# Kernel optimization log

Hardware: AMD Instinct MI355X
Metric: run time of the kernel (lower is better)

The kernel has to match this reference:

```python
import jax, jax.numpy as jnp
import numpy as np
from jax import lax

LN_EPS = 1e-5
GRN_EPS = 1e-6


def _convnext_block(x, cw, cb, lng, lnb, w1, b1, gg, gb, w2, b2):
    # x: [B, C, H, W] NCHW; cw: [C, 1, 7, 7] depthwise kernel
    dim = x.shape[1]
    y = lax.conv_general_dilated(
        x, cw, window_strides=(1, 1), padding=[(3, 3), (3, 3)],
        dimension_numbers=('NCHW', 'OIHW', 'NCHW'), feature_group_count=dim)
    y = y + cb[None, :, None, None]
    y = y.transpose(0, 2, 3, 1)  # NHWC
    # LayerNorm over channels
    mu = y.mean(-1, keepdims=True)
    var = ((y - mu) ** 2).mean(-1, keepdims=True)
    y = (y - mu) * lax.rsqrt(var + LN_EPS) * lng + lnb
    # pointwise expand
    y = y @ w1 + b1
    y = jax.nn.gelu(y, approximate=False)
    # Global Response Normalization
    gx = jnp.sqrt(jnp.sum(y * y, axis=(1, 2), keepdims=True))  # [B,1,1,C']
    nx = gx / (gx.mean(-1, keepdims=True) + GRN_EPS)
    y = gg * (y * nx) + gb + y
    # pointwise project
    y = y @ w2 + b2
    return y.transpose(0, 3, 1, 2) + x


def _stack_blocks(x, cw, cb, lng, lnb, w1, b1, gg, gb, w2, b2):
    for i in range(cw.shape[0]):
        x = _convnext_block(x, cw[i], cb[i], lng[i], lnb[i], w1[i], b1[i],
                            gg[i], gb[i], w2[i], b2[i])
    return x


def setup_inputs() -> dict:
    key = jax.random.key(0)
    B, C, H, W = 8, 256, 64, 64
    K = 1024
    INTER = 4 * C
    DEPTH = 2
    ks = jax.random.split(key, 8)
    x = jax.random.normal(ks[0], (B, C, H, W), jnp.float32)
    codebook = jax.random.uniform(ks[1], (K, C), jnp.float32, -1.0 / K, 1.0 / K)

    def make_params(k):
        k1, k2, k3 = jax.random.split(k, 3)
        return dict(
            conv_w=0.02 * jax.random.normal(k1, (DEPTH, C, 1, 7, 7), jnp.float32),
            conv_b=jnp.zeros((DEPTH, C), jnp.float32),
            ln_g=jnp.ones((DEPTH, C), jnp.float32),
            ln_b=jnp.zeros((DEPTH, C), jnp.float32),
            fc1_w=0.02 * jax.random.normal(k2, (DEPTH, C, INTER), jnp.float32),
            fc1_b=jnp.zeros((DEPTH, INTER), jnp.float32),
            grn_g=jnp.zeros((DEPTH, INTER), jnp.float32),
            grn_b=jnp.zeros((DEPTH, INTER), jnp.float32),
            fc2_w=0.02 * jax.random.normal(k3, (DEPTH, INTER, C), jnp.float32),
            fc2_b=jnp.zeros((DEPTH, C), jnp.float32),
        )

    enc = make_params(ks[2])
    dec = make_params(ks[3])
    out = {'x': x, 'codebook': codebook}
    for name, p in (('enc', enc), ('dec', dec)):
        for k2, v in p.items():
            out[f'{name}_{k2}'] = v
    return out


def reference(x, codebook,
              enc_conv_w, enc_conv_b, enc_ln_g, enc_ln_b, enc_fc1_w, enc_fc1_b,
              enc_grn_g, enc_grn_b, enc_fc2_w, enc_fc2_b,
              dec_conv_w, dec_conv_b, dec_ln_g, dec_ln_b, dec_fc1_w, dec_fc1_b,
              dec_grn_g, dec_grn_b, dec_fc2_w, dec_fc2_b):
    B, C, H, W = x.shape
    inputs = _stack_blocks(x, enc_conv_w, enc_conv_b, enc_ln_g, enc_ln_b,
                           enc_fc1_w, enc_fc1_b, enc_grn_g, enc_grn_b,
                           enc_fc2_w, enc_fc2_b)
    inputs = inputs.transpose(0, 2, 3, 1)  # [B,H,W,C]
    flat = inputs.reshape(-1, C)  # [N, C]
    # squared Euclidean distances (argmin invariant to sqrt)
    d2 = (jnp.sum(flat * flat, axis=1, keepdims=True)
          - 2.0 * (flat @ codebook.T)
          + jnp.sum(codebook * codebook, axis=1)[None, :])  # [N, K]
    encoding_indices = jnp.argmin(d2, axis=1)  # [N]
    quantized = codebook[encoding_indices].reshape(inputs.shape)  # [B,H,W,C]
    matched_indices = encoding_indices.reshape(B, H, W)
    # straight-through estimator
    quantized = lax.stop_gradient(quantized) + inputs - lax.stop_gradient(inputs)
    quantized = quantized.transpose(0, 3, 1, 2)  # [B,C,H,W]
    decoded = _stack_blocks(quantized, dec_conv_w, dec_conv_b, dec_ln_g, dec_ln_b,
                            dec_fc1_w, dec_fc1_b, dec_grn_g, dec_grn_b,
                            dec_fc2_w, dec_fc2_b)
    return quantized, decoded, matched_indices
```

## Files before the change

kernel.cpp:

```cpp
#include <hip/hip_runtime.h>
#include <math.h>
#include <stdint.h>

typedef unsigned short u16;
typedef unsigned long long u64;
typedef __attribute__((ext_vector_type(8))) short bf16x8;
typedef __attribute__((ext_vector_type(4))) float f32x4;

__device__ __forceinline__ u16 bfhi(float v) {
  unsigned u = __float_as_uint(v);
  u += 0x7FFFu + ((u >> 16) & 1u);
  return (u16)(u >> 16);
}
__device__ __forceinline__ float b2f(u16 h) { return __uint_as_float((unsigned)h << 16); }

__device__ __forceinline__ void gload16(void* lds, const void* g) {
  __builtin_amdgcn_global_load_lds(
      (const __attribute__((address_space(1))) unsigned int*)g,
      (__attribute__((address_space(3))) unsigned int*)lds, 16, 0, 0);
}

__global__ __launch_bounds__(256) void k_conv(const float* __restrict__ in,
                                              const float* __restrict__ cw,
                                              const float* __restrict__ cb,
                                              float* __restrict__ out) {
  const int bx = blockIdx.x;
  const int c = bx & 255;
  __shared__ float patch[70 * 76];
  const int t = threadIdx.x;
  const float* plane = in + (size_t)bx * 4096;
  for (int i = t; i < 1330; i += 256) {
    const int row = i / 19, cf = i - row * 19;
    const int bit = (row >> 2) & 1;
    const int gf = cf - 1 - bit;
    const int h = row - 3;
    float4 v = {0.f, 0.f, 0.f, 0.f};
    if ((unsigned)h < 64u && (unsigned)gf < 16u) v = *(const float4*)(plane + h * 64 + gf * 4);
    *(float4*)(patch + row * 76 + cf * 4) = v;
  }
  const float* wp = cw + c * 49;
  float wt[49];
#pragma unroll
  for (int i = 0; i < 49; ++i) wt[i] = wp[i];
  const float bias = cb[c];
  __syncthreads();
  const int j = t & 7, i = t >> 3;
  const int w0 = j * 8, h0 = i * 2;
  float acc[2][8];
#pragma unroll
  for (int dr = 0; dr < 2; ++dr)
#pragma unroll
    for (int ww = 0; ww < 8; ++ww) acc[dr][ww] = bias;
#pragma unroll
  for (int r = 0; r < 8; ++r) {
    const int prow = h0 + r;
    const int bit = (prow >> 2) & 1;
    const float* base = patch + prow * 76 + w0 + 4 * bit;
    float win[16];
#pragma unroll
    for (int q = 0; q < 4; ++q) {
      const float4 v = *(const float4*)(base + q * 4);
      win[q * 4 + 0] = v.x; win[q * 4 + 1] = v.y;
      win[q * 4 + 2] = v.z; win[q * 4 + 3] = v.w;
    }
#pragma unroll
    for (int dr = 0; dr < 2; ++dr) {
      const int kh = r - dr;
      if (kh >= 0 && kh < 7) {
#pragma unroll
        for (int kw = 0; kw < 7; ++kw) {
          const float wv = wt[kh * 7 + kw];
#pragma unroll
          for (int ww = 0; ww < 8; ++ww)
            acc[dr][ww] = fmaf(win[ww + kw + 1], wv, acc[dr][ww]);
        }
      }
    }
  }
  float* op = out + (size_t)bx * 4096;
#pragma unroll
  for (int dr = 0; dr < 2; ++dr) {
    const int hh = h0 + dr;
    float4 o1, o2;
    o1.x = acc[dr][0]; o1.y = acc[dr][1]; o1.z = acc[dr][2]; o1.w = acc[dr][3];
    o2.x = acc[dr][4]; o2.y = acc[dr][5]; o2.z = acc[dr][6]; o2.w = acc[dr][7];
    *(float4*)(op + hh * 64 + w0) = o1;
    *(float4*)(op + hh * 64 + w0 + 4) = o2;
  }
}

__global__ __launch_bounds__(256) void k_lnT(const float* __restrict__ src,
                                             const float* __restrict__ g,
                                             const float* __restrict__ bt,
                                             u16* __restrict__ Rh, u16* __restrict__ Rl,
                                             const int wlo) {
  __shared__ float T[256 * 33];
  __shared__ float red[8 * 32];
  __shared__ float gs[256], bs[256];
  const int t = threadIdx.x;
  const int n0 = blockIdx.x * 32;
  const int b = n0 >> 12, pl = n0 & 4095;
  gs[t] = g[t];
  bs[t] = bt[t];
  const int m = t & 7, h = t >> 3;
  const float* sp = src + (((size_t)(b * 256)) << 12) + pl + m * 4;
#pragma unroll
  for (int it = 0; it < 8; ++it) {
    const int c = it * 32 + h;
    const float4 v = *(const float4*)(sp + ((size_t)c << 12));
    *(float4*)(T + c * 33 + m * 4) = v;
  }
  __syncthreads();
  const int p = t & 31, qq = t >> 5;
  float s = 0.f;
#pragma unroll
  for (int jj = 0; jj < 32; ++jj) s += T[(qq * 32 + jj) * 33 + p];
  red[qq * 32 + p] = s;
  __syncthreads();
  float tot = 0.f;
#pragma unroll
  for (int k = 0; k < 8; ++k) tot += red[k * 32 + p];
  const float mu = tot * (1.0f / 256.0f);
  __syncthreads();
  float s2 = 0.f;
#pragma unroll
  for (int jj = 0; jj < 32; ++jj) {
    const float d = T[(qq * 32 + jj) * 33 + p] - mu;
    s2 = fmaf(d, d, s2);
  }
  red[qq * 32 + p] = s2;
  __syncthreads();
  float tot2 = 0.f;
#pragma unroll
  for (int k = 0; k < 8; ++k) tot2 += red[k * 32 + p];
  const float rs = 1.0f / sqrtf(tot2 * (1.0f / 256.0f) + 1e-5f);
#pragma unroll
  for (int jj = 0; jj < 32; ++jj) {
    const int c = qq * 32 + jj;
    const float y = (T[c * 33 + p] - mu) * rs * gs[c] + bs[c];
    const u16 hh = bfhi(y);
    const u16 ll = bfhi(y - b2f(hh));
    ((unsigned*)T)[c * 33 + p] = ((unsigned)hh << 16) | ll;
  }
  __syncthreads();
  const int w = t >> 6, l = t & 63;
  const unsigned* Tu = (const unsigned*)T;
#pragma unroll
  for (int r = 0; r < 4; ++r) {
    const int px = r * 8 + w * 2 + (l >> 5);
    const int c0 = (l & 31) * 8;
    unsigned hp[4], lp[4];
#pragma unroll
    for (int jj = 0; jj < 4; ++jj) {
      const unsigned a = Tu[(c0 + 2 * jj) * 33 + px];
      const unsigned bb = Tu[(c0 + 2 * jj + 1) * 33 + px];
      hp[jj] = (a >> 16) | (bb & 0xffff0000u);
      lp[jj] = (a & 0xffffu) | (bb << 16);
    }
    const size_t base = (size_t)(n0 + px) * 256 + c0;
    *(uint4*)(Rh + base) = make_uint4(hp[0], hp[1], hp[2], hp[3]);
    if (wlo) *(uint4*)(Rl + base) = make_uint4(lp[0], lp[1], lp[2], lp[3]);
  }
}

template <int KD, int SPLIT, int EPI>
__global__ __launch_bounds__(256) void k_gemm(
    const u16* __restrict__ Ah_, const u16* __restrict__ Al_,
    const u16* __restrict__ Bh_, const u16* __restrict__ Bl_,
    const int row0, const long long bstride,
    const float* __restrict__ pbias,
    u16* __restrict__ poh, u16* __restrict__ pol,
    float* __restrict__ pxout, const float* __restrict__ pxin,
    float* __restrict__ pgx2, u64* __restrict__ pmin) {
  constexpr int STAGE_B = (SPLIT ? 4 : 2) * 16384;
  constexpr int TRANS_B = (EPI == 1) ? 64 * 129 * 4 : 0;
  constexpr int SMEM_B = STAGE_B > TRANS_B ? STAGE_B : TRANS_B;
  __shared__ __align__(16) char smem[SMEM_B];
  u16* As_h = (u16*)smem;
  u16* As_l = (u16*)(smem + 16384);
  u16* Bs_h = (u16*)(smem + (SPLIT ? 32768 : 16384));
  u16* Bs_l = (u16*)(smem + 49152);

  const int t = threadIdx.x;
  const int w = t >> 6, l = t & 63;
  const int quad = l >> 4, lm = l & 15;
  const int wr = (w & 1) * 64, wc = (w >> 1) * 64;
  const int colt = blockIdx.x, rowt = blockIdx.y;
  const int nblk0 = rowt * 128;
  const int bglob = (row0 + nblk0) >> 12;

  const u16* Agh = Ah_ + (size_t)nblk0 * KD;
  const u16* Agl = SPLIT ? (Al_ + (size_t)nblk0 * KD) : Ah_;
  const u16* Bgh = Bh_ + (size_t)bglob * (size_t)bstride + (size_t)(colt * 128) * KD;
  const u16* Bgl = SPLIT ? (Bl_ + (size_t)bglob * (size_t)bstride + (size_t)(colt * 128) * KD) : Bh_;

  f32x4 acc[4][4];
  const f32x4 zz = {0.f, 0.f, 0.f, 0.f};
#pragma unroll
  for (int i = 0; i < 4; ++i)
#pragma unroll
    for (int j = 0; j < 4; ++j) acc[i][j] = zz;

  auto stage = [&](u16* Sp, const u16* Gp, int ks) {
#pragma unroll
    for (int ii = 0; ii < 4; ++ii) {
      const int o = ii * 4096 + t * 16;
      const int row = o >> 7;
      const int kl = (((o >> 4) & 7) ^ (row & 7)) << 3;
      gload16((char*)Sp + o, Gp + (size_t)row * KD + ks * 64 + kl);
    }
  };

#pragma unroll 1
  for (int ks = 0; ks < KD / 64; ++ks) {
    stage(As_h, Agh, ks);
    stage(Bs_h, Bgh, ks);
    if constexpr (SPLIT) {
      stage(As_l, Agl, ks);
      stage(Bs_l, Bgl, ks);
    }
    __syncthreads();
#pragma unroll
    for (int kk = 0; kk < 2; ++kk) {
      bf16x8 ah[4], bh[4];
#pragma unroll
      for (int i = 0; i < 4; ++i) {
        const int row = wr + i * 16 + lm;
        ah[i] = *(const bf16x8*)(As_h + row * 64 + (((kk * 4 + quad) ^ (row & 7)) << 3));
        const int col = wc + i * 16 + lm;
        bh[i] = *(const bf16x8*)(Bs_h + col * 64 + (((kk * 4 + quad) ^ (col & 7)) << 3));
      }
#pragma unroll
      for (int i = 0; i < 4; ++i)
#pragma unroll
        for (int j = 0; j < 4; ++j)
          acc[i][j] = __builtin_amdgcn_mfma_f32_16x16x32_bf16(ah[i], bh[j], acc[i][j], 0, 0, 0);
      if constexpr (SPLIT) {
        bf16x8 xl[4];
#pragma unroll
        for (int i = 0; i < 4; ++i) {
          const int row = wr + i * 16 + lm;
          xl[i] = *(const bf16x8*)(As_l + row * 64 + (((kk * 4 + quad) ^ (row & 7)) << 3));
        }
#pragma unroll
        for (int i = 0; i < 4; ++i)
#pragma unroll
          for (int j = 0; j < 4; ++j)
            acc[i][j] = __builtin_amdgcn_mfma_f32_16x16x32_bf16(xl[i], bh[j], acc[i][j], 0, 0, 0);
#pragma unroll
        for (int i = 0; i < 4; ++i) {
          const int col = wc + i * 16 + lm;
          xl[i] = *(const bf16x8*)(Bs_l + col * 64 + (((kk * 4 + quad) ^ (col & 7)) << 3));
        }
#pragma unroll
        for (int i = 0; i < 4; ++i)
#pragma unroll
          for (int j = 0; j < 4; ++j)
            acc[i][j] = __builtin_amdgcn_mfma_f32_16x16x32_bf16(ah[i], xl[j], acc[i][j], 0, 0, 0);
      }
    }
    __syncthreads();
  }

  if constexpr (EPI == 0) {
    float csum[4] = {0.f, 0.f, 0.f, 0.f};
    float bv[4];
#pragma unroll
    for (int j = 0; j < 4; ++j) bv[j] = pbias[colt * 128 + wc + j * 16 + lm];
#pragma unroll
    for (int i = 0; i < 4; ++i) {
#pragma unroll
      for (int r = 0; r < 4; ++r) {
        const int row = nblk0 + wr + i * 16 + quad * 4 + r;
#pragma unroll
        for (int j = 0; j < 4; ++j) {
          const int col = colt * 128 + wc + j * 16 + lm;
          const float x = acc[i][j][r] + bv[j];
          const float gl = 0.5f * x * (1.0f + erff(x * 0.70710678118654752f));
          csum[j] = fmaf(gl, gl, csum[j]);
          const size_t idx = (size_t)row * 1024 + col;
          const u16 h = bfhi(gl);
          poh[idx] = h;
          if constexpr (SPLIT) pol[idx] = bfhi(gl - b2f(h));
        }
      }
    }
#pragma unroll
    for (int j = 0; j < 4; ++j) {
      float cs = csum[j];
      cs += __shfl_xor(cs, 16);
      cs += __shfl_xor(cs, 32);
      if (quad == 0)
        unsafeAtomicAdd(&pgx2[bglob * 1024 + colt * 128 + wc + j * 16 + lm], cs);
    }
  } else if constexpr (EPI == 1) {
    float* T = (float*)smem;
    const int pg0 = (row0 + nblk0) & 4095;
    const int bb = (row0 + nblk0) >> 12;
#pragma unroll 1
    for (int h = 0; h < 2; ++h) {
      __syncthreads();
      if ((w >> 1) == h) {
#pragma unroll
        for (int i = 0; i < 4; ++i) {
          const int row = wr + i * 16 + quad * 4;
#pragma unroll
          for (int j = 0; j < 4; ++j) {
            const int cl = j * 16 + lm;
#pragma unroll
            for (int r = 0; r < 4; ++r) T[cl * 129 + row + r] = acc[i][j][r];
          }
        }
      }
      __syncthreads();
      const int lp = (l & 31) * 4;
      const int ch2 = l >> 5;
#pragma unroll
      for (int step = 0; step < 8; ++step) {
        const int cl = w * 16 + step * 2 + ch2;
        const int cg = colt * 128 + h * 64 + cl;
        float4 tv = *(float4*)&T[cl * 129 + lp];
        const float bv2 = pbias[cg];
        const size_t nchw = (((size_t)(bb * 256 + cg)) << 12) + pg0 + lp;
        const float4 xv = *(const float4*)(pxin + nchw);
        float4 z;
        z.x = tv.x + bv2 + xv.x;
        z.y = tv.y + bv2 + xv.y;
        z.z = tv.z + bv2 + xv.z;
        z.w = tv.w + bv2 + xv.w;
        if (pxout) *(float4*)(pxout + nchw) = z;
        if (poh) *(float4*)&T[cl * 129 + lp] = z;
      }
      if (poh) {
        __syncthreads();
        const int cl3 = t & 63;
        const int cg3 = colt * 128 + h * 64 + cl3;
        const int r0 = (t >> 6) * 32;
#pragma unroll
        for (int n = 0; n < 32; ++n) {
          const float z = T[cl3 * 129 + r0 + n];
          const size_t idx = (size_t)(nblk0 + r0 + n) * 256 + cg3;
          const u16 hh = bfhi(z);
          poh[idx] = hh;
          pol[idx] = bfhi(z - b2f(hh));
        }
      }
    }
  } else {
#pragma unroll
    for (int i = 0; i < 4; ++i) {
#pragma unroll
      for (int r = 0; r < 4; ++r) {
        const int nloc = nblk0 + wr + i * 16 + quad * 4 + r;
        const float tnv = pxin[nloc];
        u64 best = ~0ULL;
#pragma unroll
        for (int j = 0; j < 4; ++j) {
          const int code = colt * 128 + wc + j * 16 + lm;
          const float d = __fadd_rn(__fsub_rn(tnv, __fmul_rn(2.0f, acc[i][j][r])), pbias[code]);
          const u64 pk = (((u64)__float_as_uint(d)) << 32) | (unsigned)code;
          best = pk < best ? pk : best;
        }
#pragma unroll
        for (int off = 1; off < 16; off <<= 1) {
          unsigned lo32 = (unsigned)best, hi32 = (unsigned)(best >> 32);
          lo32 = __shfl_xor(lo32, off);
          hi32 = __shfl_xor(hi32, off);
          const u64 o2 = (((u64)hi32) << 32) | lo32;
          best = o2 < best ? o2 : best;
        }
        if (lm == 0) atomicMin(pmin + nloc, best);
      }
    }
  }
}

__global__ __launch_bounds__(256) void k_rownorm(const u16* __restrict__ Eh,
                                                 const u16* __restrict__ El,
                                                 float* __restrict__ tn) {
  const int t = threadIdx.x;
  const int r = t >> 2, p = t & 3;
  const int n = blockIdx.x * 64 + r;
  const u16* ph = Eh + (size_t)n * 256 + p * 64;
  const u16* pl = El + (size_t)n * 256 + p * 64;
  float s = 0.f;
#pragma unroll
  for (int j = 0; j < 8; ++j) {
    const uint4 hv = *(const uint4*)(ph + j * 8);
    const uint4 lv = *(const uint4*)(pl + j * 8);
    const unsigned hu[4] = {hv.x, hv.y, hv.z, hv.w};
    const unsigned lu[4] = {lv.x, lv.y, lv.z, lv.w};
#pragma unroll
    for (int q = 0; q < 4; ++q) {
      const float v0 = b2f((u16)(hu[q] & 0xffff)) + b2f((u16)(lu[q] & 0xffff));
      const float v1 = b2f((u16)(hu[q] >> 16)) + b2f((u16)(lu[q] >> 16));
      s = fmaf(v0, v0, s);
      s = fmaf(v1, v1, s);
    }
  }
  s += __shfl_xor(s, 1);
  s += __shfl_xor(s, 2);
  if (p == 0) tn[n] = s;
}

__global__ __launch_bounds__(256) void k_grn_scale(const float* __restrict__ GX2,
                                                   const float* __restrict__ gg,
                                                   float* __restrict__ S, int b0) {
  const int b = b0 + blockIdx.x, t = threadIdx.x;
  const float* gxb = GX2 + (size_t)b * 1024;
  float gx[4];
  float s = 0.f;
#pragma unroll
  for (int i = 0; i < 4; ++i) {
    gx[i] = sqrtf(gxb[t + i * 256]);
    s += gx[i];
  }
  const int w = t >> 6, l = t & 63;
#pragma unroll
  for (int o = 32; o > 0; o >>= 1) s += __shfl_down(s, o);
  __shared__ float red[4];
  __shared__ float bc;
  if (l == 0) red[w] = s;
  __syncthreads();
  if (t == 0) bc = 1.0f / ((red[0] + red[1] + red[2] + red[3]) * (1.0f / 1024.0f) + 1e-6f);
  __syncthreads();
  const float inv = bc;
#pragma unroll
  for (int i = 0; i < 4; ++i)
    S[(size_t)b * 1024 + t + i * 256] = fmaf(gg[t + i * 256], gx[i] * inv, 1.0f);
}

__global__ __launch_bounds__(256) void k_w2prep(const float* __restrict__ W2,
                                                const float* __restrict__ S, int b0,
                                                u16* __restrict__ Wh, u16* __restrict__ Wl) {
  const int bx = blockIdx.x;
  const int b = b0 + (bx >> 8), n = bx & 255;
  const int t = threadIdx.x;
#pragma unroll
  for (int j = 0; j < 4; ++j) {
    const int k = t + j * 256;
    const float v = W2[(size_t)k * 256 + n] * S[(size_t)b * 1024 + k];
    const size_t idx = ((size_t)(b * 256 + n)) * 1024 + k;
    const u16 h = bfhi(v);
    Wh[idx] = h;
    Wl[idx] = bfhi(v - b2f(h));
  }
}

__global__ __launch_bounds__(256) void k_bias2(const float* __restrict__ W2,
                                               const float* __restrict__ gb,
                                               const float* __restrict__ b2,
                                               float* __restrict__ out) {
  const int c = blockIdx.x, t = threadIdx.x;
  float acc = 0.f;
#pragma unroll
  for (int j = 0; j < 4; ++j) {
    const int k = t + j * 256;
    acc = fmaf(gb[k], W2[(size_t)k * 256 + c], acc);
  }
  const int w = t >> 6, l = t & 63;
#pragma unroll
  for (int o = 32; o > 0; o >>= 1) acc += __shfl_down(acc, o);
  __shared__ float red[4];
  if (l == 0) red[w] = acc;
  __syncthreads();
  if (t == 0) out[c] = red[0] + red[1] + red[2] + red[3] + b2[c];
}

__global__ __launch_bounds__(256) void k_wt(const float* __restrict__ W1,
                                            u16* __restrict__ Wh, u16* __restrict__ Wl) {
  const int bx = blockIdx.x;
  const int d = bx >> 10, n = bx & 1023;
  const int k = threadIdx.x;
  const float v = W1[(size_t)d * 262144 + (size_t)k * 1024 + n];
  const size_t idx = (size_t)bx * 256 + k;
  const u16 h = bfhi(v);
  Wh[idx] = h;
  Wl[idx] = bfhi(v - b2f(h));
}

__global__ __launch_bounds__(256) void k_csplit(const float* __restrict__ C,
                                                u16* __restrict__ Ch, u16* __restrict__ Cl) {
  const size_t i = (size_t)blockIdx.x * 256 + threadIdx.x;
  const float v = C[i];
  const u16 h = bfhi(v);
  Ch[i] = h;
  Cl[i] = bfhi(v - b2f(h));
}

__device__ __forceinline__ float np_pairwise_sq_256(const float* p) {
  float half[2];
#pragma unroll
  for (int hh = 0; hh < 2; ++hh) {
    float r[8];
#pragma unroll
    for (int j = 0; j < 8; ++j) {
      const float v = p[hh * 128 + j];
      r[j] = __fmul_rn(v, v);
    }
    for (int i = 8; i < 128; i += 8) {
#pragma unroll
      for (int j = 0; j < 8; ++j) {
        const float v = p[hh * 128 + i + j];
        r[j] = __fadd_rn(r[j], __fmul_rn(v, v));
      }
    }
    half[hh] = __fadd_rn(__fadd_rn(__fadd_rn(r[0], r[1]), __fadd_rn(r[2], r[3])),
                         __fadd_rn(__fadd_rn(r[4], r[5]), __fadd_rn(r[6], r[7])));
  }
  return __fadd_rn(half[0], half[1]);
}

__global__ __launch_bounds__(256) void k_c2(const float* __restrict__ cbk, float* __restrict__ c2) {
  const int k = blockIdx.x * 256 + threadIdx.x;
  c2[k] = np_pairwise_sq_256(cbk + (size_t)k * 256);
}

__global__ __launch_bounds__(256) void k_idx(const u64* __restrict__ pk, float* __restrict__ outI) {
  const int n = blockIdx.x * 256 + threadIdx.x;
  outI[n] = (float)(unsigned)(pk[n] & 0xffffffffULL);
}

__global__ __launch_bounds__(256) void k_gather(const u64* __restrict__ pk,
                                                const float* __restrict__ cbk,
                                                float* __restrict__ outq) {
  const int t = threadIdx.x;
  const int p0 = blockIdx.x * 64;
  const int b = p0 >> 12, pl = (p0 & 4095) + (t & 63);
  const int cg = t >> 6;
  const int n = p0 + (t & 63);
  const int k = (int)(unsigned)(pk[n] & 0xffffffffULL);
  const float* crow = cbk + (size_t)k * 256 + cg * 64;
  float* ob = outq + (((size_t)(b * 256 + cg * 64)) << 12) + pl;
#pragma unroll 1
  for (int j = 0; j < 16; ++j) {
    const float4 cv = *(const float4*)(crow + j * 4);
    ob[((size_t)(j * 4 + 0)) << 12] = cv.x;
    ob[((size_t)(j * 4 + 1)) << 12] = cv.y;
    ob[((size_t)(j * 4 + 2)) << 12] = cv.z;
    ob[((size_t)(j * 4 + 3)) << 12] = cv.w;
  }
}

extern "C" void kernel_launch(void* const* d_in, const int* in_sizes, int n_in,
                              void* d_out, int out_size, void* d_ws, size_t ws_size,
                              hipStream_t stream) {
  const float* x = (const float*)d_in[0];
  const float* cbk = (const float*)d_in[1];
  const float* Pe[10];
  const float* Pd[10];
  for (int i = 0; i < 10; ++i) Pe[i] = (const float*)d_in[2 + i];
  for (int i = 0; i < 10; ++i) Pd[i] = (const float*)d_in[12 + i];

  float* ws = (float*)d_ws;
  size_t o = 0;
  auto alloc = [&](size_t nf) {
    float* p = ws + o;
    o += (nf + 63) & ~(size_t)63;
    return p;
  };
  float* P1 = alloc(8388608);
  u16* Rh = (u16*)alloc(4194304);
  u16* Rl = (u16*)alloc(4194304);
  u16* W1th_e = (u16*)alloc(262144);
  u16* W1tl_e = (u16*)alloc(262144);
  u16* W1th_d = (u16*)alloc(262144);
  u16* W1tl_d = (u16*)alloc(262144);
  u16* W2sh = (u16*)alloc(1048576);
  u16* W2sl = (u16*)alloc(1048576);
  u16* Ch = (u16*)alloc(131072);
  u16* Cl = (u16*)alloc(131072);
  float* C2v = alloc(1024);
  float* GX2 = alloc(8192);
  float* Sv = alloc(8192);
  float* bias2v = alloc(256);
  float* tn = alloc(32768);
  u64* pk = (u64*)alloc(65536);
  const size_t fixedf = o;
  const size_t availf = (ws_size / 4 > fixedf) ? ws_size / 4 - fixedf : 0;
  int chunkB = (int)(availf / 4194304);
  if (chunkB > 8) chunkB = 8;
  if (chunkB < 1) chunkB = 1;
  float* Cv = ws + o;
  u16* Mh = (u16*)(ws + o);
  u16* Ml = (u16*)(ws + o + (size_t)chunkB * 2097152);

  float* outQ = (float*)d_out;
  float* outD = outQ + 8388608;
  float* outI = outD + 8388608;

  auto run_enc = [&](const float* xin, float* xout, u16* Eh, u16* El,
                     const float* const* pp, int d) {
    k_conv<<<2048, 256, 0, stream>>>(xin, pp[0] + (size_t)d * 256 * 49, pp[1] + d * 256, Cv);
    k_lnT<<<1024, 256, 0, stream>>>(Cv, pp[2] + d * 256, pp[3] + d * 256, Rh, Rl, 1);
    k_bias2<<<256, 256, 0, stream>>>(pp[8] + (size_t)d * 262144, pp[7] + d * 1024,
                                     pp[9] + d * 256, bias2v);
    hipMemsetAsync(GX2, 0, 8192 * 4, stream);
    for (int b0 = 0; b0 < 8; b0 += chunkB) {
      const int nb = (8 - b0 < chunkB) ? 8 - b0 : chunkB;
      k_gemm<256, 1, 0><<<dim3(8, nb * 32), 256, 0, stream>>>(
          Rh + (size_t)b0 * 4096 * 256, Rl + (size_t)b0 * 4096 * 256,
          W1th_e + (size_t)d * 262144, W1tl_e + (size_t)d * 262144,
          b0 * 4096, 0, Pe[5] + d * 1024, Mh, Ml, nullptr, nullptr, GX2, nullptr);
      k_grn_scale<<<nb, 256, 0, stream>>>(GX2, pp[6] + d * 1024, Sv, b0);
      k_w2prep<<<nb * 256, 256, 0, stream>>>(pp[8] + (size_t)d * 262144, Sv, b0, W2sh, W2sl);
      k_gemm<1024, 1, 1><<<dim3(2, nb * 32), 256, 0, stream>>>(
          Mh, Ml, W2sh, W2sl, b0 * 4096, 262144LL, bias2v,
          Eh ? Eh + (size_t)b0 * 4096 * 256 : (u16*)nullptr,
          El ? El + (size_t)b0 * 4096 * 256 : (u16*)nullptr,
          xout, xin, nullptr, nullptr);
    }
  };

  auto run_dec = [&](const float* xin, float* xout, const float* const* pp, int d) {
    k_conv<<<2048, 256, 0, stream>>>(xin, pp[0] + (size_t)d * 256 * 49, pp[1] + d * 256, Cv);
    k_lnT<<<1024, 256, 0, stream>>>(Cv, pp[2] + d * 256, pp[3] + d * 256, Rh, Rl, 0);
    k_bias2<<<256, 256, 0, stream>>>(pp[8] + (size_t)d * 262144, pp[7] + d * 1024,
                                     pp[9] + d * 256, bias2v);
    hipMemsetAsync(GX2, 0, 8192 * 4, stream);
    for (int b0 = 0; b0 < 8; b0 += chunkB) {
      const int nb = (8 - b0 < chunkB) ? 8 - b0 : chunkB;
      k_gemm<256, 0, 0><<<dim3(8, nb * 32), 256, 0, stream>>>(
          Rh + (size_t)b0 * 4096 * 256, nullptr,
          W1th_d + (size_t)d * 262144, nullptr,
          b0 * 4096, 0, Pd[5] + d * 1024, Mh, nullptr, nullptr, nullptr, GX2, nullptr);
      k_grn_scale<<<nb, 256, 0, stream>>>(GX2, pp[6] + d * 1024, Sv, b0);
      k_w2prep<<<nb * 256, 256, 0, stream>>>(pp[8] + (size_t)d * 262144, Sv, b0, W2sh, W2sl);
      k_gemm<1024, 0, 1><<<dim3(2, nb * 32), 256, 0, stream>>>(
          Mh, nullptr, W2sh, nullptr, b0 * 4096, 262144LL, bias2v,
          nullptr, nullptr, xout, xin, nullptr, nullptr);
    }
  };

  k_wt<<<2048, 256, 0, stream>>>(Pe[4], W1th_e, W1tl_e);
  k_wt<<<2048, 256, 0, stream>>>(Pd[4], W1th_d, W1tl_d);
  k_csplit<<<1024, 256, 0, stream>>>(cbk, Ch, Cl);
  k_c2<<<4, 256, 0, stream>>>(cbk, C2v);

  run_enc(x, P1, nullptr, nullptr, Pe, 0);
  run_enc(P1, nullptr, Rh, Rl, Pe, 1);

  k_rownorm<<<512, 256, 0, stream>>>(Rh, Rl, tn);
  hipMemsetAsync(pk, 0xFF, 32768 * 8, stream);
  k_gemm<256, 1, 2><<<dim3(8, 256), 256, 0, stream>>>(Rh, Rl, Ch, Cl, 0, 0,
                                                      C2v, nullptr, nullptr, nullptr,
                                                      tn, nullptr, pk);
  k_idx<<<128, 256, 0, stream>>>(pk, outI);
  k_gather<<<512, 256, 0, stream>>>(pk, cbk, outQ);

  run_dec(outQ, P1, Pd, 0);
  run_dec(P1, outD, Pd, 1);
}
```

Before: 1.011 ms.

## Double-buffer GEMM K-loop with 32-wide stages and swizzle block-to-tile mapping

The GEMM main loop moves from single-buffered 64-wide K stages to double-buffered 32-wide stages. Each iteration prefetches the next stage into the alternate LDS buffer while computing on the current one, and drops one barrier per iteration. It also remaps the linear block id so that groups of 8 row tiles share column tiles, aiming for better L2 reuse of the B operand. The change adds a new LDS swizzle for 64-byte rows, which brings a risk of bank conflicts, and halves the MFMA work done between barriers.

```diff
diff --git a/kernel.cpp b/kernel.cpp
--- a/kernel.cpp
+++ b/kernel.cpp
@@ -163,7 +163,7 @@
   }
 }
 
-template <int KD, int SPLIT, int EPI>
+template <int KD, int SPLIT, int EPI, int NCT>
 __global__ __launch_bounds__(256) void k_gemm(
     const u16* __restrict__ Ah_, const u16* __restrict__ Al_,
     const u16* __restrict__ Bh_, const u16* __restrict__ Bl_,
@@ -172,20 +172,21 @@
     u16* __restrict__ poh, u16* __restrict__ pol,
     float* __restrict__ pxout, const float* __restrict__ pxin,
     float* __restrict__ pgx2, u64* __restrict__ pmin) {
-  constexpr int STAGE_B = (SPLIT ? 4 : 2) * 16384;
+  constexpr int HALF_B = (SPLIT ? 4 : 2) * 8192;
+  constexpr int STAGE_B = 2 * HALF_B;
   constexpr int TRANS_B = (EPI == 1) ? 64 * 129 * 4 : 0;
   constexpr int SMEM_B = STAGE_B > TRANS_B ? STAGE_B : TRANS_B;
+  constexpr int NS = KD / 32;
   __shared__ __align__(16) char smem[SMEM_B];
-  u16* As_h = (u16*)smem;
-  u16* As_l = (u16*)(smem + 16384);
-  u16* Bs_h = (u16*)(smem + (SPLIT ? 32768 : 16384));
-  u16* Bs_l = (u16*)(smem + 49152);
 
   const int t = threadIdx.x;
   const int w = t >> 6, l = t & 63;
   const int quad = l >> 4, lm = l & 15;
   const int wr = (w & 1) * 64, wc = (w >> 1) * 64;
-  const int colt = blockIdx.x, rowt = blockIdx.y;
+  const int id = blockIdx.x + gridDim.x * blockIdx.y;
+  constexpr int L = (NCT == 8) ? 3 : 1;
+  const int colt = (id >> 3) & (NCT - 1);
+  const int rowt = (id & 7) + ((id >> (3 + L)) << 3);
   const int nblk0 = rowt * 128;
   const int bglob = (row0 + nblk0) >> 12;
 
@@ -201,63 +202,67 @@
 #pragma unroll
     for (int j = 0; j < 4; ++j) acc[i][j] = zz;
 
-  auto stage = [&](u16* Sp, const u16* Gp, int ks) {
-#pragma unroll
-    for (int ii = 0; ii < 4; ++ii) {
+  auto stage32 = [&](char* Sp, const u16* Gp, int ks) {
+#pragma unroll
+    for (int ii = 0; ii < 2; ++ii) {
       const int o = ii * 4096 + t * 16;
-      const int row = o >> 7;
-      const int kl = (((o >> 4) & 7) ^ (row & 7)) << 3;
-      gload16((char*)Sp + o, Gp + (size_t)row * KD + ks * 64 + kl);
+      const int row = o >> 6;
+      const int lc = ((o >> 4) & 3) ^ ((row ^ (row >> 2)) & 3);
+      gload16(Sp + o, Gp + (size_t)row * KD + ks * 32 + lc * 8);
     }
   };
+  auto stage_all = [&](int b, int ks) {
+    char* base = smem + (size_t)b * HALF_B;
+    stage32(base, Agh, ks);
+    stage32(base + 8192, Bgh, ks);
+    if constexpr (SPLIT) {
+      stage32(base + 16384, Agl, ks);
+      stage32(base + 24576, Bgl, ks);
+    }
+  };
+  auto frag_at = [&](const u16* S, int rc) -> bf16x8 {
+    const int sw = ((rc ^ (rc >> 2)) & 3) ^ quad;
+    return *(const bf16x8*)(S + rc * 32 + (sw << 3));
+  };
+
+  stage_all(0, 0);
+  __syncthreads();
 
 #pragma unroll 1
-  for (int ks = 0; ks < KD / 64; ++ks) {
-    stage(As_h, Agh, ks);
-    stage(Bs_h, Bgh, ks);
+  for (int ks = 0; ks < NS; ++ks) {
+    if (ks + 1 < NS) stage_all((ks + 1) & 1, ks + 1);
+    const u16* base = (const u16*)(smem + (size_t)(ks & 1) * HALF_B);
+    const u16* Ah = base;
+    const u16* Bh = base + 4096;
+    bf16x8 ah[4], bh[4];
+#pragma unroll
+    for (int i = 0; i < 4; ++i) {
+      ah[i] = frag_at(Ah, wr + i * 16 + lm);
+      bh[i] = frag_at(Bh, wc + i * 16 + lm);
+    }
+#pragma unroll
+    for (int i = 0; i < 4; ++i)
+#pragma unroll
+      for (int j = 0; j < 4; ++j)
+        acc[i][j] = __builtin_amdgcn_mfma_f32_16x16x32_bf16(ah[i], bh[j], acc[i][j], 0, 0, 0);
     if constexpr (SPLIT) {
-      stage(As_l, Agl, ks);
-      stage(Bs_l, Bgl, ks);
-    }
-    __syncthreads();
-#pragma unroll
-    for (int kk = 0; kk < 2; ++kk) {
-      bf16x8 ah[4], bh[4];
-#pragma unroll
-      for (int i = 0; i < 4; ++i) {
-        const int row = wr + i * 16 + lm;
-        ah[i] = *(const bf16x8*)(As_h + row * 64 + (((kk * 4 + quad) ^ (row & 7)) << 3));
-        const int col = wc + i * 16 + lm;
-        bh[i] = *(const bf16x8*)(Bs_h + col * 64 + (((kk * 4 + quad) ^ (col & 7)) << 3));
-      }
+      const u16* Al = base + 8192;
+      const u16* Bl = base + 12288;
+      bf16x8 xl[4];
+#pragma unroll
+      for (int i = 0; i < 4; ++i) xl[i] = frag_at(Al, wr + i * 16 + lm);
 #pragma unroll
       for (int i = 0; i < 4; ++i)
 #pragma unroll
         for (int j = 0; j < 4; ++j)
-          acc[i][j] = __builtin_amdgcn_mfma_f32_16x16x32_bf16(ah[i], bh[j], acc[i][j], 0, 0, 0);
-      if constexpr (SPLIT) {
-        bf16x8 xl[4];
-#pragma unroll
-        for (int i = 0; i < 4; ++i) {
-          const int row = wr + i * 16 + lm;
-          xl[i] = *(const bf16x8*)(As_l + row * 64 + (((kk * 4 + quad) ^ (row & 7)) << 3));
-        }
-#pragma unroll
-        for (int i = 0; i < 4; ++i)
-#pragma unroll
-          for (int j = 0; j < 4; ++j)
-            acc[i][j] = __builtin_amdgcn_mfma_f32_16x16x32_bf16(xl[i], bh[j], acc[i][j], 0, 0, 0);
-#pragma unroll
-        for (int i = 0; i < 4; ++i) {
-          const int col = wc + i * 16 + lm;
-          xl[i] = *(const bf16x8*)(Bs_l + col * 64 + (((kk * 4 + quad) ^ (col & 7)) << 3));
-        }
-#pragma unroll
-        for (int i = 0; i < 4; ++i)
-#pragma unroll
-          for (int j = 0; j < 4; ++j)
-            acc[i][j] = __builtin_amdgcn_mfma_f32_16x16x32_bf16(ah[i], xl[j], acc[i][j], 0, 0, 0);
-      }
+          acc[i][j] = __builtin_amdgcn_mfma_f32_16x16x32_bf16(xl[i], bh[j], acc[i][j], 0, 0, 0);
+#pragma unroll
+      for (int i = 0; i < 4; ++i) xl[i] = frag_at(Bl, wc + i * 16 + lm);
+#pragma unroll
+      for (int i = 0; i < 4; ++i)
+#pragma unroll
+        for (int j = 0; j < 4; ++j)
+          acc[i][j] = __builtin_amdgcn_mfma_f32_16x16x32_bf16(ah[i], xl[j], acc[i][j], 0, 0, 0);
     }
     __syncthreads();
   }
@@ -598,13 +603,13 @@
     hipMemsetAsync(GX2, 0, 8192 * 4, stream);
     for (int b0 = 0; b0 < 8; b0 += chunkB) {
       const int nb = (8 - b0 < chunkB) ? 8 - b0 : chunkB;
-      k_gemm<256, 1, 0><<<dim3(8, nb * 32), 256, 0, stream>>>(
+      k_gemm<256, 1, 0, 8><<<dim3(8, nb * 32), 256, 0, stream>>>(
           Rh + (size_t)b0 * 4096 * 256, Rl + (size_t)b0 * 4096 * 256,
           W1th_e + (size_t)d * 262144, W1tl_e + (size_t)d * 262144,
           b0 * 4096, 0, Pe[5] + d * 1024, Mh, Ml, nullptr, nullptr, GX2, nullptr);
       k_grn_scale<<<nb, 256, 0, stream>>>(GX2, pp[6] + d * 1024, Sv, b0);
       k_w2prep<<<nb * 256, 256, 0, stream>>>(pp[8] + (size_t)d * 262144, Sv, b0, W2sh, W2sl);
-      k_gemm<1024, 1, 1><<<dim3(2, nb * 32), 256, 0, stream>>>(
+      k_gemm<1024, 1, 1, 2><<<dim3(2, nb * 32), 256, 0, stream>>>(
           Mh, Ml, W2sh, W2sl, b0 * 4096, 262144LL, bias2v,
           Eh ? Eh + (size_t)b0 * 4096 * 256 : (u16*)nullptr,
           El ? El + (size_t)b0 * 4096 * 256 : (u16*)nullptr,
@@ -620,13 +625,13 @@
     hipMemsetAsync(GX2, 0, 8192 * 4, stream);
     for (int b0 = 0; b0 < 8; b0 += chunkB) {
       const int nb = (8 - b0 < chunkB) ? 8 - b0 : chunkB;
-      k_gemm<256, 0, 0><<<dim3(8, nb * 32), 256, 0, stream>>>(
+      k_gemm<256, 0, 0, 8><<<dim3(8, nb * 32), 256, 0, stream>>>(
           Rh + (size_t)b0 * 4096 * 256, nullptr,
           W1th_d + (size_t)d * 262144, nullptr,
           b0 * 4096, 0, Pd[5] + d * 1024, Mh, nullptr, nullptr, nullptr, GX2, nullptr);
       k_grn_scale<<<nb, 256, 0, stream>>>(GX2, pp[6] + d * 1024, Sv, b0);
       k_w2prep<<<nb * 256, 256, 0, stream>>>(pp[8] + (size_t)d * 262144, Sv, b0, W2sh, W2sl);
-      k_gemm<1024, 0, 1><<<dim3(2, nb * 32), 256, 0, stream>>>(
+      k_gemm<1024, 0, 1, 2><<<dim3(2, nb * 32), 256, 0, stream>>>(
           Mh, nullptr, W2sh, nullptr, b0 * 4096, 262144LL, bias2v,
           nullptr, nullptr, xout, xin, nullptr, nullptr);
     }
@@ -642,9 +647,9 @@
 
   k_rownorm<<<512, 256, 0, stream>>>(Rh, Rl, tn);
   hipMemsetAsync(pk, 0xFF, 32768 * 8, stream);
-  k_gemm<256, 1, 2><<<dim3(8, 256), 256, 0, stream>>>(Rh, Rl, Ch, Cl, 0, 0,
-                                                      C2v, nullptr, nullptr, nullptr,
-                                                      tn, nullptr, pk);
+  k_gemm<256, 1, 2, 8><<<dim3(8, 256), 256, 0, stream>>>(Rh, Rl, Ch, Cl, 0, 0,
+                                                         C2v, nullptr, nullptr, nullptr,
+                                                         tn, nullptr, pk);
   k_idx<<<128, 256, 0, stream>>>(pk, outI);
   k_gather<<<512, 256, 0, stream>>>(pk, cbk, outQ);
 
```

Result: faster. 985.8 us (-2.5%).
